# Optimization experiments

Measured on AMD Instinct MI355X. Metric: run time of the kernel, lower is better.

Reference implementation:

```python
import jax, jax.numpy as jnp
import numpy as np

EPS = 1e-8
TINY = 1e-12
C_L1 = float(np.sqrt(3.0 / (4.0 * np.pi)))  # integral-normalized l=1 SH coefficient


def _elu_feature_map(x):
    # positive_feature_map(kind='elu'): elu(x) + 1 > 0
    return jax.nn.elu(x) + 1.0


def _sph_bessel_j1(x):
    # j1(x) = sin(x)/x^2 - cos(x)/x, with series x/3 near 0 for stability
    small = x < 1e-4
    xs = jnp.where(small, 1.0, x)
    return jnp.where(small, x / 3.0, jnp.sin(xs) / (xs * xs) - jnp.cos(xs) / xs)


def setup_inputs() -> dict:
    key = jax.random.key(0)
    k1, k2, k3, k4, k5 = jax.random.split(key, 5)
    B, N, H, D, C, Q = 1, 2048, 8, 32, 32, 8
    pos = jax.random.normal(k1, (B, N, 3), dtype=jnp.float32) * 5.0
    q = jax.random.normal(k2, (B, N, H, D), dtype=jnp.float32)
    k = jax.random.normal(k3, (B, N, H, D), dtype=jnp.float32)
    v = jax.random.normal(k4, (B, N, H, C), dtype=jnp.float32)
    kappa = jnp.linspace(0.5, 4.0, Q, dtype=jnp.float32)          # (Q,) buffer
    a = jax.random.normal(k5, (H, Q), dtype=jnp.float32) * 0.1    # (H,Q) -> 'head' mode
    node_mask = jnp.ones((B, N), dtype=bool)
    return {"pos": pos, "q": q, "k": k, "v": v, "kappa": kappa, "a": a, "node_mask": node_mask}


def reference(pos, q, k, v, kappa, a, node_mask):
    B, N = pos.shape[0], pos.shape[1]
    m = node_mask.astype(pos.dtype)  # (B,N)

    # Linear (kernel) attention: alpha[b,h,i,j] = <phi(q_i), phi(k_j)> / sum_n <phi(q_i), phi(k_n)>
    phi_q = _elu_feature_map(q) * m[:, :, None, None]
    phi_k = _elu_feature_map(k) * m[:, :, None, None]
    v_m = v * m[:, :, None, None]
    logits = jnp.einsum('bihd,bjhd->bhij', phi_q, phi_k)
    denom = jnp.maximum(logits.sum(axis=-1, keepdims=True), EPS)
    alpha = logits / denom  # (B,H,N,N)

    # Pairwise geometry
    r_ij = pos[:, :, None, :] - pos[:, None, :, :]            # (B,N,N,3)
    dist = jnp.sqrt(jnp.sum(r_ij * r_ij, axis=-1) + TINY)     # (B,N,N)
    eye = jnp.eye(N, dtype=bool)
    safe_vec = jnp.array([1.0, 0.0, 0.0], dtype=pos.dtype)
    r_safe = jnp.where(eye[None, :, :, None], safe_vec, r_ij)

    # Real spherical harmonics, l=1, integral normalization, on normalized r_ij
    rn = jnp.sqrt(jnp.sum(r_safe * r_safe, axis=-1, keepdims=True) + TINY)
    Y = C_L1 * (r_safe / rn)  # (B,N,N,3) -> M=3 components

    # Radial part: f[b,h,i,j] = sum_q a[h,q] * j1(dist_ij * kappa_q)
    x = dist[..., None] * kappa  # (B,N,N,Q)
    jl = _sph_bessel_j1(x)
    f = jnp.einsum('bijq,hq->bhij', jl, a)

    # out[b,i,h,m,c] = sum_j alpha*f * Y * v
    w = alpha * f
    out = jnp.einsum('bhij,bijm,bjhc->bihmc', w, Y, v_m)
    return out  # (B, N, H, 2l+1=3, C)
```

## Files before the change

### kernel.cpp

```cpp
#include <hip/hip_runtime.h>

#define NN   2048
#define NH   8
#define ND   32
#define NC   32
#define NQ   8
#define JS   8
#define NOUT (NN*NH*3*NC)
#define EPSV 1e-8f
#define TINYV 1e-12f
#define C_L1 0.4886025119029199f
#define PSCALE 128.0f

typedef _Float16 half8 __attribute__((ext_vector_type(8)));
typedef __fp16   fp16x2 __attribute__((ext_vector_type(2)));
typedef float    f32x4 __attribute__((ext_vector_type(4)));
typedef float    f32x2 __attribute__((ext_vector_type(2)));

__device__ __forceinline__ float phi_elu(float x) { return x > 0.f ? x + 1.f : __expf(x); }
__device__ __forceinline__ float rfl(float x) {
    return __int_as_float(__builtin_amdgcn_readfirstlane(__float_as_int(x)));
}
__device__ __forceinline__ void glds16(const void* g, void* l) {
    __builtin_amdgcn_global_load_lds(
        (const __attribute__((address_space(1))) void*)g,
        (__attribute__((address_space(3))) void*)l, 16, 0, 0);
}

__global__ __launch_bounds__(256)
void k_prep(const float* __restrict__ pos, const float* __restrict__ q,
            const float* __restrict__ k, const float* __restrict__ v,
            _Float16* __restrict__ phiQ16, _Float16* __restrict__ KtF,
            _Float16* __restrict__ VtF, float* __restrict__ posT,
            float* __restrict__ ksum) {
    __shared__ __align__(16) char smem[33280];
    int b = blockIdx.x, t = threadIdx.x;
    int wid = t >> 6, lane = t & 63;
    if (b < 64) {
        _Float16* lds_k = (_Float16*)smem;
        int jblk = b;
        #pragma unroll 4
        for (int jj = 0; jj < 32; ++jj) {
            int j = jblk * 32 + jj;
            float pq = phi_elu(q[j * 256 + t]);
            float pk = phi_elu(k[j * 256 + t]);
            phiQ16[j * 256 + t] = (_Float16)pq;
            lds_k[jj * 264 + t] = (_Float16)pk;
        }
        __syncthreads();
        float s = 0.f;
        #pragma unroll
        for (int jj = 0; jj < 32; ++jj) s += (float)lds_k[jj * 264 + t];
        atomicAdd(&ksum[t], s);
        int lo = lane & 15, dg = lane >> 4;
        #pragma unroll
        for (int uu = 0; uu < 4; ++uu) {
            int unit = wid * 4 + uu;
            int h = unit >> 1, jf = unit & 1;
            half8 kf = *(const half8*)&lds_k[(jf * 16 + lo) * 264 + h * 32 + dg * 8];
            ((half8*)KtF)[(size_t)((h * 64 + jblk) * 2 + jf) * 64 + lane] = kf;
        }
    } else {
        float* lds_v = (float*)smem;
        float* lds_p = (float*)(smem + 32768);
        int jblk = b - 64;
        #pragma unroll 4
        for (int jj = 0; jj < 32; ++jj)
            lds_v[jj * 256 + t] = v[(size_t)(jblk * 32 + jj) * 256 + t];
        if (t < 96) lds_p[t] = pos[jblk * 96 + t];
        __syncthreads();
        if (t < 96) {
            int m = t >> 5, jj = t & 31;
            posT[m * NN + jblk * 32 + jj] = lds_p[jj * 3 + m];
        }
        int li = lane & 15, g8 = lane >> 4;
        #pragma unroll
        for (int uu = 0; uu < 16; ++uu) {
            int unit = wid * 16 + uu;
            int hgrp = unit >> 4, pl = (unit >> 2) & 3, hh = (unit >> 1) & 1, cf = unit & 1;
            int h = hgrp * 2 + hh, c = cf * 16 + li;
            half8 w;
            #pragma unroll
            for (int e = 0; e < 8; ++e) {
                int jl = g8 * 4 + (e & 3) + 16 * (e >> 2);
                float vv = lds_v[jl * 256 + h * 32 + c];
                float fac = (pl == 0) ? 1.f : lds_p[jl * 3 + (pl - 1)];
                w[e] = (_Float16)(vv * fac);
            }
            ((half8*)VtF)[((size_t)(jblk * 4 + hgrp) * 16 + pl * 4 + hh * 2 + cf) * 64 + lane] = w;
        }
    }
}

__global__ void k_coef(const float* __restrict__ kappa, const float* __restrict__ a,
                       float* __restrict__ coef) {
    int t = threadIdx.x;
    if (t >= NH) return;
    float An[8];
    #pragma unroll
    for (int n = 0; n < 8; ++n) An[n] = a[t * NQ + n];
    float k0 = kappa[0];
    float ik0 = 1.f / k0, ik02 = ik0 * ik0;
    const float Tc[9][9] = {
        {0,0,0,0,0,0,0,0,0},
        {0,1,0,0,0,0,0,0,0},
        {-1,0,2,0,0,0,0,0,0},
        {0,-3,0,4,0,0,0,0,0},
        {1,0,-8,0,8,0,0,0,0},
        {0,5,0,-20,0,16,0,0,0},
        {-1,0,18,0,-48,0,32,0,0},
        {0,-7,0,56,0,-112,0,64,0},
        {1,0,-32,0,160,0,-256,0,128}};
    const float Uc[9][8] = {
        {0,0,0,0,0,0,0,0},
        {1,0,0,0,0,0,0,0},
        {0,2,0,0,0,0,0,0},
        {-1,0,4,0,0,0,0,0},
        {0,-4,0,8,0,0,0,0},
        {1,0,-12,0,16,0,0,0},
        {0,6,0,-32,0,32,0,0},
        {-1,0,24,0,-80,0,64,0},
        {0,-8,0,80,0,-192,0,128}};
    #pragma unroll
    for (int kk = 0; kk < 9; ++kk) {
        float s = 0.f;
        #pragma unroll
        for (int n = 1; n <= 8; ++n) s = fmaf(An[n-1] * (1.f / n), Tc[n][kk], s);
        coef[kk * 8 + t] = s * ik0;
    }
    #pragma unroll
    for (int kk = 0; kk < 8; ++kk) {
        float s = 0.f;
        #pragma unroll
        for (int n = 1; n <= 8; ++n) s = fmaf(An[n-1] * (1.f / (n * n)), Uc[n][kk], s);
        coef[(9 + kk) * 8 + t] = s * ik02;
    }
}

__global__ __launch_bounds__(256, 3)
void k_main(const float* __restrict__ posT, const _Float16* __restrict__ phiQ16,
            const _Float16* __restrict__ KtF, const _Float16* __restrict__ VtF,
            const float* __restrict__ kappa, const float* __restrict__ coef,
            const float* __restrict__ ksum, _Float16* __restrict__ part) {
    __shared__ __align__(16) char smem[2 * 16384];
    int tid = threadIdx.x;
    int wid = tid >> 6, lane = tid & 63;
    int li = lane & 15, g = lane >> 4;

    int bid = blockIdx.x;
    int hgrp = bid & 3, js = (bid >> 2) & 7, ib = bid >> 5;
    int itile = ib * 64 + wid * 16;

    float k0 = rfl(kappa[0]);

    float pc0[2];
    f32x2 cpq[2][8];
    #pragma unroll
    for (int hh = 0; hh < 2; ++hh) {
        int h = hgrp * 2 + hh;
        pc0[hh] = rfl(coef[h]);
        cpq[hh][0][0] = rfl(coef[8 * 8 + h]);
        cpq[hh][0][1] = rfl(coef[(9 + 7) * 8 + h]);
        #pragma unroll
        for (int kk = 1; kk <= 7; ++kk) {
            cpq[hh][kk][0] = rfl(coef[kk * 8 + h]);
            cpq[hh][kk][1] = rfl(coef[(9 + kk - 1) * 8 + h]);
        }
    }

    half8 qa[2];
    #pragma unroll
    for (int hh = 0; hh < 2; ++hh)
        qa[hh] = ((const half8*)phiQ16)[((size_t)(itile + li) * NH + hgrp * 2 + hh) * 4 + g];

    float pi0 = posT[itile + li];
    float pi1 = posT[NN + itile + li];
    float pi2 = posT[2 * NN + itile + li];

    f32x4 acc[2][4][2];
    #pragma unroll
    for (int hh = 0; hh < 2; ++hh)
      #pragma unroll
      for (int pl = 0; pl < 4; ++pl)
        #pragma unroll
        for (int cf = 0; cf < 2; ++cf)
          acc[hh][pl][cf] = (f32x4){0.f, 0.f, 0.f, 0.f};

    const int j0 = js * (NN / JS);
    const int NCHUNK = (NN / JS) / 32;
    const f32x4 z4 = (f32x4){0.f, 0.f, 0.f, 0.f};
    const int soff = wid * 4096 + lane * 16;

    {
        size_t sl = (size_t)((j0 >> 5) * 4 + hgrp);
        const char* src = (const char*)VtF + (sl << 14) + soff;
        char* dstl = smem + soff;
        #pragma unroll
        for (int kk = 0; kk < 4; ++kk)
            glds16(src + kk * 1024, dstl + kk * 1024);
    }

    #pragma unroll 1
    for (int t = 0; t < NCHUNK; ++t) {
        int jc = j0 + t * 32, jblk = jc >> 5;

        union { half8 h; fp16x2 p[4]; } wa[2];

        #pragma unroll
        for (int jF = 0; jF < 2; ++jF) {
            f32x4 pj4[3];
            #pragma unroll
            for (int m = 0; m < 3; ++m)
                pj4[m] = *(const f32x4*)(posT + m * NN + jc + jF * 16 + g * 4);

            f32x4 s[2];
            #pragma unroll
            for (int hh = 0; hh < 2; ++hh) {
                int h = hgrp * 2 + hh;
                half8 kf = ((const half8*)KtF)[(size_t)((h * 64 + jblk) * 2 + jF) * 64 + lane];
                s[hh] = __builtin_amdgcn_mfma_f32_16x16x32_f16(kf, qa[hh], z4, 0, 0, 0);
            }

            float gux[2][4];
            #pragma unroll
            for (int r = 0; r < 4; ++r) {
                float dx = pi0 - pj4[0][r];
                float dy = pi1 - pj4[1][r];
                float dz = pi2 - pj4[2][r];
                float d2 = fmaf(dx, dx, fmaf(dy, dy, fmaf(dz, dz, TINYV)));
                float u = rsqrtf(d2);
                u = (d2 < 1e-10f) ? 0.f : u;
                float dist = d2 * u;
                float th = dist * k0;
                float sth, cth;
                __sincosf(th, &sth, &cth);
                float e1 = u * u;
                float ws = u * sth;
                f32x2 cc; cc[0] = cth; cc[1] = cth;
                #pragma unroll
                for (int hh = 0; hh < 2; ++hh) {
                    f32x2 pq = cpq[hh][0];
                    #pragma unroll
                    for (int kk = 7; kk >= 1; --kk)
                        pq = __builtin_elementwise_fma(pq, cc, cpq[hh][kk]);
                    float P = fmaf(pq[0], cth, pc0[hh]);
                    float inner = fmaf(ws, pq[1], -P);
                    gux[hh][r] = (s[hh][r] * e1) * inner;
                }
            }
            #pragma unroll
            for (int hh = 0; hh < 2; ++hh) {
                wa[hh].p[jF * 2 + 0] = __builtin_amdgcn_cvt_pkrtz(gux[hh][0], gux[hh][1]);
                wa[hh].p[jF * 2 + 1] = __builtin_amdgcn_cvt_pkrtz(gux[hh][2], gux[hh][3]);
            }
        }

        __syncthreads();

        const char* vb = smem + (t & 1) * 16384;
        #pragma unroll
        for (int hh = 0; hh < 2; ++hh) {
            #pragma unroll
            for (int pl = 0; pl < 4; ++pl) {
                half8 vf0 = *(const half8*)(vb + ((pl * 4 + hh * 2 + 0) * 1024) + lane * 16);
                half8 vf1 = *(const half8*)(vb + ((pl * 4 + hh * 2 + 1) * 1024) + lane * 16);
                acc[hh][pl][0] = __builtin_amdgcn_mfma_f32_16x16x32_f16(wa[hh].h, vf0, acc[hh][pl][0], 0, 0, 0);
                acc[hh][pl][1] = __builtin_amdgcn_mfma_f32_16x16x32_f16(wa[hh].h, vf1, acc[hh][pl][1], 0, 0, 0);
            }
        }

        if (t + 1 < NCHUNK) {
            size_t sl = (size_t)((jblk + 1) * 4 + hgrp);
            const char* src = (const char*)VtF + (sl << 14) + soff;
            char* dstl = smem + ((t + 1) & 1) * 16384 + soff;
            #pragma unroll
            for (int kk = 0; kk < 4; ++kk)
                glds16(src + kk * 1024, dstl + kk * 1024);
        }
    }

    f32x4 pi_ep[3];
    #pragma unroll
    for (int m = 0; m < 3; ++m)
        pi_ep[m] = *(const f32x4*)(posT + m * NN + itile + g * 4);

    float dinvC[2][4];
    #pragma unroll
    for (int hh = 0; hh < 2; ++hh) {
        int h = hgrp * 2 + hh;
        float p = 0.f;
        #pragma unroll
        for (int e = 0; e < 8; ++e) p += (float)qa[hh][e] * ksum[h * 32 + g * 8 + e];
        p += __shfl_xor(p, 16);
        p += __shfl_xor(p, 32);
        float dcol = (C_L1 * PSCALE) / fmaxf(p, EPSV);
        #pragma unroll
        for (int r = 0; r < 4; ++r)
            dinvC[hh][r] = __shfl(dcol, g * 4 + r);
    }

    _Float16* pdst = part + (size_t)js * NOUT;
    #pragma unroll
    for (int hh = 0; hh < 2; ++hh) {
        int h = hgrp * 2 + hh;
        #pragma unroll
        for (int m = 0; m < 3; ++m)
        #pragma unroll
        for (int cf = 0; cf < 2; ++cf)
        #pragma unroll
        for (int r = 0; r < 4; ++r) {
            int i = itile + g * 4 + r;
            size_t idx = ((size_t)i * NH + h) * 96 + m * 32 + cf * 16 + li;
            float val = fmaf(pi_ep[m][r], acc[hh][0][cf][r], -acc[hh][m + 1][cf][r]);
            pdst[idx] = (_Float16)(val * dinvC[hh][r]);
        }
    }
}

__global__ void k_reduce(const _Float16* __restrict__ part, float4* __restrict__ out) {
    int e = blockIdx.x * 256 + threadIdx.x;
    const int NO8 = NOUT / 8;
    if (e >= NO8) return;
    float s[8] = {0.f, 0.f, 0.f, 0.f, 0.f, 0.f, 0.f, 0.f};
    #pragma unroll
    for (int p = 0; p < JS; ++p) {
        half8 t = ((const half8*)part)[(size_t)p * NO8 + e];
        #pragma unroll
        for (int x = 0; x < 8; ++x) s[x] += (float)t[x];
    }
    const float S = 1.f / PSCALE;
    out[e * 2]     = make_float4(s[0] * S, s[1] * S, s[2] * S, s[3] * S);
    out[e * 2 + 1] = make_float4(s[4] * S, s[5] * S, s[6] * S, s[7] * S);
}

extern "C" void kernel_launch(void* const* d_in, const int* in_sizes, int n_in,
                              void* d_out, int out_size, void* d_ws, size_t ws_size,
                              hipStream_t stream) {
    const float* pos   = (const float*)d_in[0];
    const float* q     = (const float*)d_in[1];
    const float* k     = (const float*)d_in[2];
    const float* v     = (const float*)d_in[3];
    const float* kappa = (const float*)d_in[4];
    const float* a     = (const float*)d_in[5];
    float* out = (float*)d_out;
    char* ws = (char*)d_ws;

    _Float16* phiQ16 = (_Float16*)(ws + 0);
    _Float16* KtF    = (_Float16*)(ws + (1u << 20));
    _Float16* VtF    = (_Float16*)(ws + (2u << 20));
    float*    posT   = (float*)   (ws + (6u << 20));
    float*    ksum   = (float*)   (ws + (6u << 20) + 24576);
    float*    coefb  = (float*)   (ws + (6u << 20) + 91136);
    _Float16* partb  = (_Float16*)(ws + (6u << 20) + 131072);

    (void)hipMemsetAsync(ksum, 0, 256 * sizeof(float), stream);
    k_prep<<<128, 256, 0, stream>>>(pos, q, k, v, phiQ16, KtF, VtF, posT, ksum);
    k_coef<<<1, 64, 0, stream>>>(kappa, a, coefb);
    k_main<<<(NN / 64) * 4 * JS, 256, 0, stream>>>(posT, phiQ16, KtF, VtF,
                                                   kappa, coefb, ksum, partb);
    k_reduce<<<(NOUT / 8 + 255) / 256, 256, 0, stream>>>(partb, (float4*)out);
}
```

Baseline: 65.99 us.

## Stage K fragments through LDS with V, merge coef kernel into prep

Changes the KtF layout so each j-block and head-group chunk is contiguous, then loads K fragments asynchronously into the double-buffered LDS alongside V instead of reading them from global memory directly in the inner loop. The prefetch of the next chunk moves to the top of the loop after a barrier so it overlaps the current chunk's compute. The coefficient kernel is folded into k_prep as an extra block, removing one launch. The LDS footprint grows, which may reduce occupancy, and the prefetch destination address uses a convoluted expression that simplifies to the intended offset.

```diff
diff --git a/kernel.cpp b/kernel.cpp
--- a/kernel.cpp
+++ b/kernel.cpp
@@ -30,9 +30,10 @@
 __global__ __launch_bounds__(256)
 void k_prep(const float* __restrict__ pos, const float* __restrict__ q,
             const float* __restrict__ k, const float* __restrict__ v,
+            const float* __restrict__ kappa, const float* __restrict__ a,
             _Float16* __restrict__ phiQ16, _Float16* __restrict__ KtF,
             _Float16* __restrict__ VtF, float* __restrict__ posT,
-            float* __restrict__ ksum) {
+            float* __restrict__ ksum, float* __restrict__ coef) {
     __shared__ __align__(16) char smem[33280];
     int b = blockIdx.x, t = threadIdx.x;
     int wid = t >> 6, lane = t & 63;
@@ -58,9 +59,9 @@
             int unit = wid * 4 + uu;
             int h = unit >> 1, jf = unit & 1;
             half8 kf = *(const half8*)&lds_k[(jf * 16 + lo) * 264 + h * 32 + dg * 8];
-            ((half8*)KtF)[(size_t)((h * 64 + jblk) * 2 + jf) * 64 + lane] = kf;
-        }
-    } else {
+            ((half8*)KtF)[((size_t)(jblk * 4 + (h >> 1)) * 4 + (h & 1) * 2 + jf) * 64 + lane] = kf;
+        }
+    } else if (b < 128) {
         float* lds_v = (float*)smem;
         float* lds_p = (float*)(smem + 32768);
         int jblk = b - 64;
@@ -89,51 +90,48 @@
             }
             ((half8*)VtF)[((size_t)(jblk * 4 + hgrp) * 16 + pl * 4 + hh * 2 + cf) * 64 + lane] = w;
         }
-    }
-}
-
-__global__ void k_coef(const float* __restrict__ kappa, const float* __restrict__ a,
-                       float* __restrict__ coef) {
-    int t = threadIdx.x;
-    if (t >= NH) return;
-    float An[8];
-    #pragma unroll
-    for (int n = 0; n < 8; ++n) An[n] = a[t * NQ + n];
-    float k0 = kappa[0];
-    float ik0 = 1.f / k0, ik02 = ik0 * ik0;
-    const float Tc[9][9] = {
-        {0,0,0,0,0,0,0,0,0},
-        {0,1,0,0,0,0,0,0,0},
-        {-1,0,2,0,0,0,0,0,0},
-        {0,-3,0,4,0,0,0,0,0},
-        {1,0,-8,0,8,0,0,0,0},
-        {0,5,0,-20,0,16,0,0,0},
-        {-1,0,18,0,-48,0,32,0,0},
-        {0,-7,0,56,0,-112,0,64,0},
-        {1,0,-32,0,160,0,-256,0,128}};
-    const float Uc[9][8] = {
-        {0,0,0,0,0,0,0,0},
-        {1,0,0,0,0,0,0,0},
-        {0,2,0,0,0,0,0,0},
-        {-1,0,4,0,0,0,0,0},
-        {0,-4,0,8,0,0,0,0},
-        {1,0,-12,0,16,0,0,0},
-        {0,6,0,-32,0,32,0,0},
-        {-1,0,24,0,-80,0,64,0},
-        {0,-8,0,80,0,-192,0,128}};
-    #pragma unroll
-    for (int kk = 0; kk < 9; ++kk) {
-        float s = 0.f;
-        #pragma unroll
-        for (int n = 1; n <= 8; ++n) s = fmaf(An[n-1] * (1.f / n), Tc[n][kk], s);
-        coef[kk * 8 + t] = s * ik0;
-    }
-    #pragma unroll
-    for (int kk = 0; kk < 8; ++kk) {
-        float s = 0.f;
-        #pragma unroll
-        for (int n = 1; n <= 8; ++n) s = fmaf(An[n-1] * (1.f / (n * n)), Uc[n][kk], s);
-        coef[(9 + kk) * 8 + t] = s * ik02;
+    } else {
+        if (t < NH) {
+            float An[8];
+            #pragma unroll
+            for (int n = 0; n < 8; ++n) An[n] = a[t * NQ + n];
+            float k0 = kappa[0];
+            float ik0 = 1.f / k0, ik02 = ik0 * ik0;
+            const float Tc[9][9] = {
+                {0,0,0,0,0,0,0,0,0},
+                {0,1,0,0,0,0,0,0,0},
+                {-1,0,2,0,0,0,0,0,0},
+                {0,-3,0,4,0,0,0,0,0},
+                {1,0,-8,0,8,0,0,0,0},
+                {0,5,0,-20,0,16,0,0,0},
+                {-1,0,18,0,-48,0,32,0,0},
+                {0,-7,0,56,0,-112,0,64,0},
+                {1,0,-32,0,160,0,-256,0,128}};
+            const float Uc[9][8] = {
+                {0,0,0,0,0,0,0,0},
+                {1,0,0,0,0,0,0,0},
+                {0,2,0,0,0,0,0,0},
+                {-1,0,4,0,0,0,0,0},
+                {0,-4,0,8,0,0,0,0},
+                {1,0,-12,0,16,0,0,0},
+                {0,6,0,-32,0,32,0,0},
+                {-1,0,24,0,-80,0,64,0},
+                {0,-8,0,80,0,-192,0,128}};
+            #pragma unroll
+            for (int kk = 0; kk < 9; ++kk) {
+                float s = 0.f;
+                #pragma unroll
+                for (int n = 1; n <= 8; ++n) s = fmaf(An[n-1] * (1.f / n), Tc[n][kk], s);
+                coef[kk * 8 + t] = s * ik0;
+            }
+            #pragma unroll
+            for (int kk = 0; kk < 8; ++kk) {
+                float s = 0.f;
+                #pragma unroll
+                for (int n = 1; n <= 8; ++n) s = fmaf(An[n-1] * (1.f / (n * n)), Uc[n][kk], s);
+                coef[(9 + kk) * 8 + t] = s * ik02;
+            }
+        }
     }
 }
 
@@ -142,7 +140,7 @@
             const _Float16* __restrict__ KtF, const _Float16* __restrict__ VtF,
             const float* __restrict__ kappa, const float* __restrict__ coef,
             const float* __restrict__ ksum, _Float16* __restrict__ part) {
-    __shared__ __align__(16) char smem[2 * 16384];
+    __shared__ __align__(16) char smem[2 * 20480];
     int tid = threadIdx.x;
     int wid = tid >> 6, lane = tid & 63;
     int li = lane & 15, g = lane >> 4;
@@ -189,20 +187,35 @@
     const int j0 = js * (NN / JS);
     const int NCHUNK = (NN / JS) / 32;
     const f32x4 z4 = (f32x4){0.f, 0.f, 0.f, 0.f};
-    const int soff = wid * 4096 + lane * 16;
+    const int koff = wid * 1024 + lane * 16;
+    const int voff = wid * 4096 + lane * 16;
 
     {
         size_t sl = (size_t)((j0 >> 5) * 4 + hgrp);
-        const char* src = (const char*)VtF + (sl << 14) + soff;
-        char* dstl = smem + soff;
+        glds16((const char*)KtF + (sl << 12) + koff, smem + koff);
+        const char* vsrc = (const char*)VtF + (sl << 14) + voff;
+        char* vd = smem + 4096 + voff;
         #pragma unroll
         for (int kk = 0; kk < 4; ++kk)
-            glds16(src + kk * 1024, dstl + kk * 1024);
+            glds16(vsrc + kk * 1024, vd + kk * 1024);
     }
 
     #pragma unroll 1
     for (int t = 0; t < NCHUNK; ++t) {
         int jc = j0 + t * 32, jblk = jc >> 5;
+        char* cb = smem + (t & 1) * 20480;
+
+        __syncthreads();
+
+        if (t + 1 < NCHUNK) {
+            size_t sl = (size_t)((jblk + 1) * 4 + hgrp);
+            char* nb = smem + ((t + 1) & 1) * 20480;
+            glds16((const char*)KtF + (sl << 12) + koff, nb + koff);
+            const char* vsrc = (const char*)VtF + (sl << 14) + voff;
+            #pragma unroll
+            for (int kk = 0; kk < 4; ++kk)
+                glds16(vsrc + kk * 1024, nb + 4096 + voff - (wid * 4096 + lane * 16) + voff + kk * 1024 - kk * 1024 + kk * 1024);
+        }
 
         union { half8 h; fp16x2 p[4]; } wa[2];
 
@@ -216,8 +229,7 @@
             f32x4 s[2];
             #pragma unroll
             for (int hh = 0; hh < 2; ++hh) {
-                int h = hgrp * 2 + hh;
-                half8 kf = ((const half8*)KtF)[(size_t)((h * 64 + jblk) * 2 + jF) * 64 + lane];
+                half8 kf = *(const half8*)(cb + (hh * 2 + jF) * 1024 + lane * 16);
                 s[hh] = __builtin_amdgcn_mfma_f32_16x16x32_f16(kf, qa[hh], z4, 0, 0, 0);
             }
 
@@ -257,7 +269,7 @@
 
         __syncthreads();
 
-        const char* vb = smem + (t & 1) * 16384;
+        const char* vb = cb + 4096;
         #pragma unroll
         for (int hh = 0; hh < 2; ++hh) {
             #pragma unroll
@@ -267,15 +279,6 @@
                 acc[hh][pl][0] = __builtin_amdgcn_mfma_f32_16x16x32_f16(wa[hh].h, vf0, acc[hh][pl][0], 0, 0, 0);
                 acc[hh][pl][1] = __builtin_amdgcn_mfma_f32_16x16x32_f16(wa[hh].h, vf1, acc[hh][pl][1], 0, 0, 0);
             }
-        }
-
-        if (t + 1 < NCHUNK) {
-            size_t sl = (size_t)((jblk + 1) * 4 + hgrp);
-            const char* src = (const char*)VtF + (sl << 14) + soff;
-            char* dstl = smem + ((t + 1) & 1) * 16384 + soff;
-            #pragma unroll
-            for (int kk = 0; kk < 4; ++kk)
-                glds16(src + kk * 1024, dstl + kk * 1024);
         }
     }
 
@@ -354,8 +357,8 @@
     _Float16* partb  = (_Float16*)(ws + (6u << 20) + 131072);
 
     (void)hipMemsetAsync(ksum, 0, 256 * sizeof(float), stream);
-    k_prep<<<128, 256, 0, stream>>>(pos, q, k, v, phiQ16, KtF, VtF, posT, ksum);
-    k_coef<<<1, 64, 0, stream>>>(kappa, a, coefb);
+    k_prep<<<129, 256, 0, stream>>>(pos, q, k, v, kappa, a,
+                                    phiQ16, KtF, VtF, posT, ksum, coefb);
     k_main<<<(NN / 64) * 4 * JS, 256, 0, stream>>>(posT, phiQ16, KtF, VtF,
                                                    kappa, coefb, ksum, partb);
     k_reduce<<<(NOUT / 8 + 255) / 256, 256, 0, stream>>>(partb, (float4*)out);
```

Result: faster. 62.77 us (-4.9%).
